# Optimization experiments

Hardware: AMD Instinct MI355X
Metric: run time of the kernel (lower is better)

## Reference

```python
import jax, jax.numpy as jnp
import numpy as np
import math

B, S, CIN, H, W = 8, 8, 64, 32, 32
COUT, K = 128, 3
PW = COUT * CIN * K * K  # 73728
P = PW + COUT            # 73856


def setup_inputs() -> dict:
    key = jax.random.key(0)
    ks = jax.random.split(key, 6)
    return {
        "x": jax.random.normal(ks[0], (B, S, CIN, H, W), dtype=jnp.float32),
        "e": jax.random.normal(ks[1], (S, P), dtype=jnp.float32),
        "mu_w": jax.random.normal(ks[2], (PW,), dtype=jnp.float32) * 0.02,
        "rho_w": jax.random.normal(ks[3], (PW,), dtype=jnp.float32) * 0.5,
        "mu_b": jax.random.normal(ks[4], (COUT,), dtype=jnp.float32) * 0.02,
        "rho_b": jax.random.normal(ks[5], (COUT,), dtype=jnp.float32) * 0.5,
    }


def _unit_log_mfg(v):
    # v: [s_n, D]; -log(2*pi)*D/2 - sum(v**2)/2  (scalar, matching torch code)
    two_pi = jnp.asarray(2.0 * math.pi, v.dtype)
    return -jnp.log(two_pi) * (v.shape[1] / 2.0) - jnp.sum(v * v) / 2.0


def reference(x, e, mu_w, rho_w, mu_b, rho_b):
    s_n = e.shape[0]
    cout = mu_b.shape[0]
    cin = x.shape[2]
    k = int(round(math.sqrt(mu_w.shape[0] / (cout * cin))))
    pw = mu_w.shape[0]

    sig_w = jax.nn.softplus(rho_w)  # log(1+exp(rho))
    sig_b = jax.nn.softplus(rho_b)
    w = mu_w[None, :] + sig_w[None, :] * e[:, :pw]          # [s_n, PW]
    b = mu_b[None, :] + sig_b[None, :] * e[:, pw:pw + cout]  # [s_n, COUT]

    entropy_q = jnp.sum(jnp.log(sig_w)) + jnp.sum(jnp.log(sig_b))
    cross_entropy_qp = _unit_log_mfg(w) + _unit_log_mfg(b)
    kl_qp = -entropy_q - cross_entropy_qp

    w5 = w.reshape(s_n, cout, cin, k, k)  # per-sample OIHW kernels

    # per-sample conv: vmap over the sample axis j; batch conv over data axis i
    def conv_one(xj, wj):  # xj [B,CIN,H,W], wj [COUT,CIN,K,K]
        return jax.lax.conv(xj, wj, (1, 1), 'VALID')

    out = jax.vmap(conv_one, in_axes=(1, 0), out_axes=1)(x, w5)  # [B,S,COUT,H',W']
    out = out + b[None, :, :, None, None]
    return out, kl_qp
```

## Files before the change

kernel.cpp:

```cpp
#include <hip/hip_runtime.h>
#include <hip/hip_bf16.h>
#include <math.h>

#define Bn    8
#define Sn    8
#define COUTc 128
#define PWc   73728
#define Pc    73856
#define WOc   30
#define NPIX  900
#define GPIX  7200
#define NSTEP 9
#define TILE  128
#define NT2   57

typedef __bf16 bf16;
typedef bf16  bf16x8 __attribute__((ext_vector_type(8)));
typedef float f32x16 __attribute__((ext_vector_type(16)));

__device__ __forceinline__ float softplus_f(float x) {
    return fmaxf(x, 0.f) + log1pf(expf(-fabsf(x)));
}

__device__ __forceinline__ unsigned int pack2(float a, float b) {
    unsigned short ua = __builtin_bit_cast(unsigned short, (bf16)a);
    unsigned short ub = __builtin_bit_cast(unsigned short, (bf16)b);
    return ((unsigned int)ub << 16) | (unsigned int)ua;
}

__device__ __forceinline__ void gl16(const void* g, void* l) {
    typedef __attribute__((address_space(1))) void gvoid;
    typedef __attribute__((address_space(3))) void lvoid;
    __builtin_amdgcn_global_load_lds((gvoid*)g, (lvoid*)l, 16, 0, 0);
}

__global__ __launch_bounds__(256) void prep_all(
        const float* __restrict__ xg, const float* __restrict__ e,
        const float* __restrict__ mu_w, const float* __restrict__ rho_w,
        const float* __restrict__ mu_b, const float* __restrict__ rho_b,
        bf16* __restrict__ xt, bf16* __restrict__ wimg,
        float* __restrict__ bq, float* __restrict__ slots) {
    const int bid = blockIdx.x;
    const int t   = threadIdx.x;

    if (bid < 512) {
        const int img  = bid >> 3;
        const int part = bid & 7;
        const int p    = part * 128 + (t >> 1);
        const int half = t & 1;
        const float* src = xg + ((size_t)img << 16) + (size_t)(half * 32) * 1024 + p;
        bf16*        dst = xt + ((size_t)img << 16) + (size_t)p * 64 + half * 32;
        #pragma unroll
        for (int o = 0; o < 4; ++o) {
            uint4 pk;
            pk.x = pack2(src[(o * 8 + 0) * 1024], src[(o * 8 + 1) * 1024]);
            pk.y = pack2(src[(o * 8 + 2) * 1024], src[(o * 8 + 3) * 1024]);
            pk.z = pack2(src[(o * 8 + 4) * 1024], src[(o * 8 + 5) * 1024]);
            pk.w = pack2(src[(o * 8 + 6) * 1024], src[(o * 8 + 7) * 1024]);
            *reinterpret_cast<uint4*>(dst + o * 8) = pk;
        }
        return;
    }

    float ls = 0.f, sq = 0.f;
    if (bid < 800) {
        const int rb    = bid - 512;
        const int r     = rb >> 5;
        const int chunk = rb & 31;
        const int idx   = chunk * 256 + t;
        const int co    = idx >> 6;
        const int ci    = idx & 63;
        const int p     = co * 576 + ci * 9 + r;
        float sig = softplus_f(rho_w[p]);
        ls = logf(sig);
        float mu = mu_w[p];
        const int dstp = (co << 6) + (((ci >> 3) ^ (co & 7)) << 3) + (ci & 7);
        #pragma unroll
        for (int s = 0; s < Sn; ++s) {
            float wv = fmaf(sig, e[s * Pc + p], mu);
            wimg[((s * NSTEP + r) << 13) + dstp] = (bf16)wv;
            sq += wv * wv;
        }
    } else {
        if (t < COUTc) {
            float sig = softplus_f(rho_b[t]);
            ls = logf(sig);
            float mu = mu_b[t];
            #pragma unroll
            for (int s = 0; s < Sn; ++s) {
                float bv = fmaf(sig, e[s * Pc + PWc + t], mu);
                bq[s * COUTc + t] = bv;
                sq += bv * bv;
            }
        }
    }

    #pragma unroll
    for (int off = 32; off > 0; off >>= 1) {
        ls += __shfl_down(ls, off);
        sq += __shfl_down(sq, off);
    }
    __shared__ float sls[4], ssq[4];
    const int lane = t & 63, wd = t >> 6;
    if (lane == 0) { sls[wd] = ls; ssq[wd] = sq; }
    __syncthreads();
    if (t == 0) {
        slots[2 * (bid - 512)]     = sls[0] + sls[1] + sls[2] + sls[3];
        slots[2 * (bid - 512) + 1] = ssq[0] + ssq[1] + ssq[2] + ssq[3];
    }
}

__global__ __launch_bounds__(256) void conv_mfma(
        const bf16* __restrict__ xt, const bf16* __restrict__ wimg,
        const float* __restrict__ bq, const float* __restrict__ slots,
        float* __restrict__ out, float* __restrict__ klout) {
    const int bid  = blockIdx.x;
    const int s    = bid & 7;
    const int tile = bid >> 3;
    const int t    = threadIdx.x;
    const int lane = t & 63;
    const int w    = t >> 6;
    const int wr   = w >> 1;
    const int wc   = w & 1;

    __shared__ bf16 Wbuf[2][8192];
    __shared__ bf16 Xbuf[2][8192];

    const char* wsrcL = (const char*)wimg + ((size_t)(s * NSTEP) << 14)
                      + (w << 12) + (lane << 4);

    const char *x0, *x1, *x2, *x3;
    #pragma unroll
    for (int q = 0; q < 4; ++q) {
        int pix = w * 32 + q * 8 + (lane >> 3);
        int g   = tile * TILE + pix;
        if (g >= GPIX) g = GPIX - 1;
        int b2 = g / NPIX;
        int rr = g - b2 * NPIX;
        int oy = rr / WOc;
        int ox = rr - oy * WOc;
        int m  = (lane & 7) ^ (pix & 7);
        const char* ptr = (const char*)xt
            + ((((size_t)(b2 * Sn + s) << 10) + oy * 32 + ox) << 7) + (m << 4);
        if (q == 0) x0 = ptr; else if (q == 1) x1 = ptr;
        else if (q == 2) x2 = ptr; else x3 = ptr;
    }

    f32x16 acc[2][2];
    #pragma unroll
    for (int i = 0; i < 2; ++i)
        #pragma unroll
        for (int j = 0; j < 2; ++j)
            #pragma unroll
            for (int k = 0; k < 16; ++k)
                acc[i][j][k] = 0.f;

    #define STAGE(stepc, b)                                                  \
    {                                                                        \
        const char* ws_ = wsrcL + ((stepc) << 14);                           \
        char* wl_ = (char*)(&Wbuf[(b)][0]) + (w << 12);                      \
        gl16(ws_,        wl_);                                               \
        gl16(ws_ + 1024, wl_ + 1024);                                        \
        gl16(ws_ + 2048, wl_ + 2048);                                        \
        gl16(ws_ + 3072, wl_ + 3072);                                        \
        const int roff_ = (((stepc) / 3) * 32 + ((stepc) % 3)) * 128;        \
        char* xl_ = (char*)(&Xbuf[(b)][0]) + (w << 12);                      \
        gl16(x0 + roff_, xl_);                                               \
        gl16(x1 + roff_, xl_ + 1024);                                        \
        gl16(x2 + roff_, xl_ + 2048);                                        \
        gl16(x3 + roff_, xl_ + 3072);                                        \
    }

    #define COMPUTE(b)                                                       \
    {                                                                        \
        const bf16* Wl_ = &Wbuf[(b)][0];                                     \
        const bf16* Xl_ = &Xbuf[(b)][0];                                     \
        _Pragma("unroll")                                                    \
        for (int kc = 0; kc < 4; ++kc) {                                     \
            const int oct_ = ((kc << 1) + (lane >> 5)) ^ (lane & 7);         \
            bf16x8 af0 = *reinterpret_cast<const bf16x8*>(                   \
                Wl_ + ((wr * 64 + (lane & 31)) << 6) + (oct_ << 3));         \
            bf16x8 af1 = *reinterpret_cast<const bf16x8*>(                   \
                Wl_ + ((wr * 64 + 32 + (lane & 31)) << 6) + (oct_ << 3));    \
            bf16x8 bf0 = *reinterpret_cast<const bf16x8*>(                   \
                Xl_ + ((wc * 64 + (lane & 31)) << 6) + (oct_ << 3));         \
            bf16x8 bf1 = *reinterpret_cast<const bf16x8*>(                   \
                Xl_ + ((wc * 64 + 32 + (lane & 31)) << 6) + (oct_ << 3));    \
            acc[0][0] = __builtin_amdgcn_mfma_f32_32x32x16_bf16(af0, bf0, acc[0][0], 0, 0, 0); \
            acc[0][1] = __builtin_amdgcn_mfma_f32_32x32x16_bf16(af0, bf1, acc[0][1], 0, 0, 0); \
            acc[1][0] = __builtin_amdgcn_mfma_f32_32x32x16_bf16(af1, bf0, acc[1][0], 0, 0, 0); \
            acc[1][1] = __builtin_amdgcn_mfma_f32_32x32x16_bf16(af1, bf1, acc[1][1], 0, 0, 0); \
        }                                                                    \
    }

    STAGE(0, 0);
    STAGE(1, 1);

    #define ITER(tt, b)                                                      \
        asm volatile("s_waitcnt vmcnt(8)" ::: "memory");                     \
        __builtin_amdgcn_s_barrier();                                        \
        __builtin_amdgcn_sched_barrier(0);                                   \
        COMPUTE(b);                                                          \
        __builtin_amdgcn_sched_barrier(0);                                   \
        __builtin_amdgcn_s_barrier();                                        \
        STAGE((tt) + 2, b);

    ITER(0, 0)
    ITER(1, 1)
    ITER(2, 0)
    ITER(3, 1)
    ITER(4, 0)
    ITER(5, 1)
    ITER(6, 0)
    asm volatile("s_waitcnt vmcnt(8)" ::: "memory");
    __builtin_amdgcn_s_barrier();
    __builtin_amdgcn_sched_barrier(0);
    COMPUTE(1);
    asm volatile("s_waitcnt vmcnt(0)" ::: "memory");
    __builtin_amdgcn_s_barrier();
    __builtin_amdgcn_sched_barrier(0);
    COMPUTE(0);

    #undef ITER
    #undef COMPUTE
    #undef STAGE

    const int colp = lane & 31;
    const int hi   = lane >> 5;
    #pragma unroll
    for (int ti = 0; ti < 2; ++ti) {
        float bs[16];
        #pragma unroll
        for (int reg = 0; reg < 16; ++reg) {
            int co = wr * 64 + ti * 32 + (reg & 3) + 8 * (reg >> 2) + 4 * hi;
            bs[reg] = bq[s * COUTc + co];
        }
        #pragma unroll
        for (int tj = 0; tj < 2; ++tj) {
            int gg = tile * TILE + wc * 64 + tj * 32 + colp;
            if (gg >= GPIX) continue;
            int b2 = gg / NPIX;
            int r2 = gg - b2 * NPIX;
            float* ob = out + (size_t)(b2 * Sn + s) * (COUTc * NPIX) + r2;
            #pragma unroll
            for (int reg = 0; reg < 16; ++reg) {
                int co = wr * 64 + ti * 32 + (reg & 3) + 8 * (reg >> 2) + 4 * hi;
                ob[co * NPIX] = acc[ti][tj][reg] + bs[reg];
            }
        }
    }

    if (bid == 0 && w == 0) {
        float ls = 0.f, sq = 0.f;
        for (int i = lane; i < 289; i += 64) {
            ls += slots[2 * i];
            sq += slots[2 * i + 1];
        }
        #pragma unroll
        for (int off = 32; off > 0; off >>= 1) {
            ls += __shfl_down(ls, off);
            sq += __shfl_down(sq, off);
        }
        if (lane == 0)
            *klout = -ls + 0.91893853320467274f * (float)Pc + 0.5f * sq;
    }
}

extern "C" void kernel_launch(void* const* d_in, const int* in_sizes, int n_in,
                              void* d_out, int out_size, void* d_ws, size_t ws_size,
                              hipStream_t stream) {
    const float* x     = (const float*)d_in[0];
    const float* e     = (const float*)d_in[1];
    const float* mu_w  = (const float*)d_in[2];
    const float* rho_w = (const float*)d_in[3];
    const float* mu_b  = (const float*)d_in[4];
    const float* rho_b = (const float*)d_in[5];
    float* out = (float*)d_out;

    bf16*  wimg  = (bf16*)d_ws;
    float* bq    = (float*)((char*)d_ws + 1179648);
    float* slots = (float*)((char*)d_ws + 1183744);
    bf16*  xt    = (bf16*)((char*)d_ws + 1187840);

    prep_all<<<dim3(801), dim3(256), 0, stream>>>(
        x, e, mu_w, rho_w, mu_b, rho_b, xt, wimg, bq, slots);

    conv_mfma<<<dim3(NT2 * Sn), dim3(256), 0, stream>>>(
        xt, wimg, bq, slots, out, out + (out_size - 1));
}
```

Measured before the change: 30.23 us.

## Use two waves per conv block with larger per-wave tiles; batch weight prep per thread

```diff
diff --git a/kernel.cpp b/kernel.cpp
--- a/kernel.cpp
+++ b/kernel.cpp
@@ -63,23 +63,28 @@
     }
 
     float ls = 0.f, sq = 0.f;
-    if (bid < 800) {
-        const int rb    = bid - 512;
-        const int r     = rb >> 5;
-        const int chunk = rb & 31;
-        const int idx   = chunk * 256 + t;
-        const int co    = idx >> 6;
-        const int ci    = idx & 63;
-        const int p     = co * 576 + ci * 9 + r;
-        float sig = softplus_f(rho_w[p]);
-        ls = logf(sig);
-        float mu = mu_w[p];
+    if (bid < 544) {
+        const int gidx = (bid - 512) * 256 + t;
+        const int co   = gidx >> 6;
+        const int ci   = gidx & 63;
+        const int p0   = co * 576 + ci * 9;
+        float mu[9], sg[9];
+        #pragma unroll
+        for (int r = 0; r < 9; ++r) {
+            mu[r] = mu_w[p0 + r];
+            sg[r] = softplus_f(rho_w[p0 + r]);
+            ls   += logf(sg[r]);
+        }
         const int dstp = (co << 6) + (((ci >> 3) ^ (co & 7)) << 3) + (ci & 7);
         #pragma unroll
         for (int s = 0; s < Sn; ++s) {
-            float wv = fmaf(sig, e[s * Pc + p], mu);
-            wimg[((s * NSTEP + r) << 13) + dstp] = (bf16)wv;
-            sq += wv * wv;
+            const float* es = e + s * Pc + p0;
+            #pragma unroll
+            for (int r = 0; r < 9; ++r) {
+                float wv = fmaf(sg[r], es[r], mu[r]);
+                wimg[((s * NSTEP + r) << 13) + dstp] = (bf16)wv;
+                sq += wv * wv;
+            }
         }
     } else {
         if (t < COUTc) {
@@ -110,7 +115,7 @@
     }
 }
 
-__global__ __launch_bounds__(256) void conv_mfma(
+__global__ __launch_bounds__(128) void conv_mfma(
         const bf16* __restrict__ xt, const bf16* __restrict__ wimg,
         const float* __restrict__ bq, const float* __restrict__ slots,
         float* __restrict__ out, float* __restrict__ klout) {
@@ -120,19 +125,17 @@
     const int t    = threadIdx.x;
     const int lane = t & 63;
     const int w    = t >> 6;
-    const int wr   = w >> 1;
-    const int wc   = w & 1;
 
     __shared__ bf16 Wbuf[2][8192];
     __shared__ bf16 Xbuf[2][8192];
 
     const char* wsrcL = (const char*)wimg + ((size_t)(s * NSTEP) << 14)
-                      + (w << 12) + (lane << 4);
-
-    const char *x0, *x1, *x2, *x3;
-    #pragma unroll
-    for (int q = 0; q < 4; ++q) {
-        int pix = w * 32 + q * 8 + (lane >> 3);
+                      + (w << 13) + (lane << 4);
+
+    const char* xs[8];
+    #pragma unroll
+    for (int q = 0; q < 8; ++q) {
+        int pix = w * 64 + q * 8 + (lane >> 3);
         int g   = tile * TILE + pix;
         if (g >= GPIX) g = GPIX - 1;
         int b2 = g / NPIX;
@@ -140,17 +143,15 @@
         int oy = rr / WOc;
         int ox = rr - oy * WOc;
         int m  = (lane & 7) ^ (pix & 7);
-        const char* ptr = (const char*)xt
+        xs[q] = (const char*)xt
             + ((((size_t)(b2 * Sn + s) << 10) + oy * 32 + ox) << 7) + (m << 4);
-        if (q == 0) x0 = ptr; else if (q == 1) x1 = ptr;
-        else if (q == 2) x2 = ptr; else x3 = ptr;
-    }
-
-    f32x16 acc[2][2];
+    }
+
+    f32x16 acc[2][4];
     #pragma unroll
     for (int i = 0; i < 2; ++i)
         #pragma unroll
-        for (int j = 0; j < 2; ++j)
+        for (int j = 0; j < 4; ++j)
             #pragma unroll
             for (int k = 0; k < 16; ++k)
                 acc[i][j][k] = 0.f;
@@ -158,17 +159,15 @@
     #define STAGE(stepc, b)                                                  \
     {                                                                        \
         const char* ws_ = wsrcL + ((stepc) << 14);                           \
-        char* wl_ = (char*)(&Wbuf[(b)][0]) + (w << 12);                      \
-        gl16(ws_,        wl_);                                               \
-        gl16(ws_ + 1024, wl_ + 1024);                                        \
-        gl16(ws_ + 2048, wl_ + 2048);                                        \
-        gl16(ws_ + 3072, wl_ + 3072);                                        \
+        char* wl_ = (char*)(&Wbuf[(b)][0]) + (w << 13);                      \
+        _Pragma("unroll")                                                    \
+        for (int q = 0; q < 8; ++q)                                          \
+            gl16(ws_ + (q << 10), wl_ + (q << 10));                          \
         const int roff_ = (((stepc) / 3) * 32 + ((stepc) % 3)) * 128;        \
-        char* xl_ = (char*)(&Xbuf[(b)][0]) + (w << 12);                      \
-        gl16(x0 + roff_, xl_);                                               \
-        gl16(x1 + roff_, xl_ + 1024);                                        \
-        gl16(x2 + roff_, xl_ + 2048);                                        \
-        gl16(x3 + roff_, xl_ + 3072);                                        \
+        char* xl_ = (char*)(&Xbuf[(b)][0]) + (w << 13);                      \
+        _Pragma("unroll")                                                    \
+        for (int q = 0; q < 8; ++q)                                          \
+            gl16(xs[q] + roff_, xl_ + (q << 10));                            \
     }
 
     #define COMPUTE(b)                                                       \
@@ -178,18 +177,26 @@
         _Pragma("unroll")                                                    \
         for (int kc = 0; kc < 4; ++kc) {                                     \
             const int oct_ = ((kc << 1) + (lane >> 5)) ^ (lane & 7);         \
-            bf16x8 af0 = *reinterpret_cast<const bf16x8*>(                   \
-                Wl_ + ((wr * 64 + (lane & 31)) << 6) + (oct_ << 3));         \
-            bf16x8 af1 = *reinterpret_cast<const bf16x8*>(                   \
-                Wl_ + ((wr * 64 + 32 + (lane & 31)) << 6) + (oct_ << 3));    \
-            bf16x8 bf0 = *reinterpret_cast<const bf16x8*>(                   \
-                Xl_ + ((wc * 64 + (lane & 31)) << 6) + (oct_ << 3));         \
-            bf16x8 bf1 = *reinterpret_cast<const bf16x8*>(                   \
-                Xl_ + ((wc * 64 + 32 + (lane & 31)) << 6) + (oct_ << 3));    \
-            acc[0][0] = __builtin_amdgcn_mfma_f32_32x32x16_bf16(af0, bf0, acc[0][0], 0, 0, 0); \
-            acc[0][1] = __builtin_amdgcn_mfma_f32_32x32x16_bf16(af0, bf1, acc[0][1], 0, 0, 0); \
-            acc[1][0] = __builtin_amdgcn_mfma_f32_32x32x16_bf16(af1, bf0, acc[1][0], 0, 0, 0); \
-            acc[1][1] = __builtin_amdgcn_mfma_f32_32x32x16_bf16(af1, bf1, acc[1][1], 0, 0, 0); \
+            bf16x8 a0 = *reinterpret_cast<const bf16x8*>(                    \
+                Wl_ + ((w * 64 + (lane & 31)) << 6) + (oct_ << 3));          \
+            bf16x8 a1 = *reinterpret_cast<const bf16x8*>(                    \
+                Wl_ + ((w * 64 + 32 + (lane & 31)) << 6) + (oct_ << 3));     \
+            bf16x8 b0 = *reinterpret_cast<const bf16x8*>(                    \
+                Xl_ + (((lane & 31)) << 6) + (oct_ << 3));                   \
+            bf16x8 b1 = *reinterpret_cast<const bf16x8*>(                    \
+                Xl_ + ((32 + (lane & 31)) << 6) + (oct_ << 3));              \
+            bf16x8 b2 = *reinterpret_cast<const bf16x8*>(                    \
+                Xl_ + ((64 + (lane & 31)) << 6) + (oct_ << 3));              \
+            bf16x8 b3 = *reinterpret_cast<const bf16x8*>(                    \
+                Xl_ + ((96 + (lane & 31)) << 6) + (oct_ << 3));              \
+            acc[0][0] = __builtin_amdgcn_mfma_f32_32x32x16_bf16(a0, b0, acc[0][0], 0, 0, 0); \
+            acc[0][1] = __builtin_amdgcn_mfma_f32_32x32x16_bf16(a0, b1, acc[0][1], 0, 0, 0); \
+            acc[0][2] = __builtin_amdgcn_mfma_f32_32x32x16_bf16(a0, b2, acc[0][2], 0, 0, 0); \
+            acc[0][3] = __builtin_amdgcn_mfma_f32_32x32x16_bf16(a0, b3, acc[0][3], 0, 0, 0); \
+            acc[1][0] = __builtin_amdgcn_mfma_f32_32x32x16_bf16(a1, b0, acc[1][0], 0, 0, 0); \
+            acc[1][1] = __builtin_amdgcn_mfma_f32_32x32x16_bf16(a1, b1, acc[1][1], 0, 0, 0); \
+            acc[1][2] = __builtin_amdgcn_mfma_f32_32x32x16_bf16(a1, b2, acc[1][2], 0, 0, 0); \
+            acc[1][3] = __builtin_amdgcn_mfma_f32_32x32x16_bf16(a1, b3, acc[1][3], 0, 0, 0); \
         }                                                                    \
     }
 
@@ -197,7 +204,7 @@
     STAGE(1, 1);
 
     #define ITER(tt, b)                                                      \
-        asm volatile("s_waitcnt vmcnt(8)" ::: "memory");                     \
+        asm volatile("s_waitcnt vmcnt(16)" ::: "memory");                    \
         __builtin_amdgcn_s_barrier();                                        \
         __builtin_amdgcn_sched_barrier(0);                                   \
         COMPUTE(b);                                                          \
@@ -212,7 +219,7 @@
     ITER(4, 0)
     ITER(5, 1)
     ITER(6, 0)
-    asm volatile("s_waitcnt vmcnt(8)" ::: "memory");
+    asm volatile("s_waitcnt vmcnt(16)" ::: "memory");
     __builtin_amdgcn_s_barrier();
     __builtin_amdgcn_sched_barrier(0);
     COMPUTE(1);
@@ -228,31 +235,31 @@
     const int colp = lane & 31;
     const int hi   = lane >> 5;
     #pragma unroll
-    for (int ti = 0; ti < 2; ++ti) {
+    for (int i = 0; i < 2; ++i) {
         float bs[16];
         #pragma unroll
         for (int reg = 0; reg < 16; ++reg) {
-            int co = wr * 64 + ti * 32 + (reg & 3) + 8 * (reg >> 2) + 4 * hi;
+            int co = w * 64 + i * 32 + (reg & 3) + 8 * (reg >> 2) + 4 * hi;
             bs[reg] = bq[s * COUTc + co];
         }
         #pragma unroll
-        for (int tj = 0; tj < 2; ++tj) {
-            int gg = tile * TILE + wc * 64 + tj * 32 + colp;
+        for (int j = 0; j < 4; ++j) {
+            int gg = tile * TILE + j * 32 + colp;
             if (gg >= GPIX) continue;
             int b2 = gg / NPIX;
             int r2 = gg - b2 * NPIX;
             float* ob = out + (size_t)(b2 * Sn + s) * (COUTc * NPIX) + r2;
             #pragma unroll
             for (int reg = 0; reg < 16; ++reg) {
-                int co = wr * 64 + ti * 32 + (reg & 3) + 8 * (reg >> 2) + 4 * hi;
-                ob[co * NPIX] = acc[ti][tj][reg] + bs[reg];
+                int co = w * 64 + i * 32 + (reg & 3) + 8 * (reg >> 2) + 4 * hi;
+                ob[co * NPIX] = acc[i][j][reg] + bs[reg];
             }
         }
     }
 
     if (bid == 0 && w == 0) {
         float ls = 0.f, sq = 0.f;
-        for (int i = lane; i < 289; i += 64) {
+        for (int i = lane; i < 33; i += 64) {
             ls += slots[2 * i];
             sq += slots[2 * i + 1];
         }
@@ -282,9 +289,9 @@
     float* slots = (float*)((char*)d_ws + 1183744);
     bf16*  xt    = (bf16*)((char*)d_ws + 1187840);
 
-    prep_all<<<dim3(801), dim3(256), 0, stream>>>(
+    prep_all<<<dim3(545), dim3(256), 0, stream>>>(
         x, e, mu_w, rho_w, mu_b, rho_b, xt, wimg, bq, slots);
 
-    conv_mfma<<<dim3(NT2 * Sn), dim3(256), 0, stream>>>(
+    conv_mfma<<<dim3(NT2 * Sn), dim3(128), 0, stream>>>(
         xt, wimg, bq, slots, out, out + (out_size - 1));
 }
```

Result: slower. 35.17 us (+16.4%).

## Halve conv pixel tile and merge weight-prep taps into fewer blocks

Applied to the files above, without the earlier changes.

```diff
diff --git a/kernel.cpp b/kernel.cpp
--- a/kernel.cpp
+++ b/kernel.cpp
@@ -11,8 +11,8 @@
 #define NPIX  900
 #define GPIX  7200
 #define NSTEP 9
-#define TILE  128
-#define NT2   57
+#define TILE  64
+#define NTIL  113
 
 typedef __bf16 bf16;
 typedef bf16  bf16x8 __attribute__((ext_vector_type(8)));
@@ -63,23 +63,28 @@
     }
 
     float ls = 0.f, sq = 0.f;
-    if (bid < 800) {
-        const int rb    = bid - 512;
-        const int r     = rb >> 5;
-        const int chunk = rb & 31;
-        const int idx   = chunk * 256 + t;
-        const int co    = idx >> 6;
-        const int ci    = idx & 63;
-        const int p     = co * 576 + ci * 9 + r;
-        float sig = softplus_f(rho_w[p]);
-        ls = logf(sig);
-        float mu = mu_w[p];
+    if (bid < 544) {
+        const int gidx = (bid - 512) * 256 + t;
+        const int co   = gidx >> 6;
+        const int ci   = gidx & 63;
+        const int p0   = co * 576 + ci * 9;
+        float mu[9], sg[9];
+        #pragma unroll
+        for (int r = 0; r < 9; ++r) {
+            mu[r] = mu_w[p0 + r];
+            sg[r] = softplus_f(rho_w[p0 + r]);
+            ls   += logf(sg[r]);
+        }
         const int dstp = (co << 6) + (((ci >> 3) ^ (co & 7)) << 3) + (ci & 7);
         #pragma unroll
         for (int s = 0; s < Sn; ++s) {
-            float wv = fmaf(sig, e[s * Pc + p], mu);
-            wimg[((s * NSTEP + r) << 13) + dstp] = (bf16)wv;
-            sq += wv * wv;
+            const float* es = e + s * Pc + p0;
+            #pragma unroll
+            for (int r = 0; r < 9; ++r) {
+                float wv = fmaf(sg[r], es[r], mu[r]);
+                wimg[((s * NSTEP + r) << 13) + dstp] = (bf16)wv;
+                sq += wv * wv;
+            }
         }
     } else {
         if (t < COUTc) {
@@ -124,36 +129,30 @@
     const int wc   = w & 1;
 
     __shared__ bf16 Wbuf[2][8192];
-    __shared__ bf16 Xbuf[2][8192];
+    __shared__ bf16 Xbuf[2][4096];
 
     const char* wsrcL = (const char*)wimg + ((size_t)(s * NSTEP) << 14)
                       + (w << 12) + (lane << 4);
 
-    const char *x0, *x1, *x2, *x3;
+    const char *x0, *x1;
     #pragma unroll
-    for (int q = 0; q < 4; ++q) {
-        int pix = w * 32 + q * 8 + (lane >> 3);
+    for (int q = 0; q < 2; ++q) {
+        int pix = w * 16 + q * 8 + (lane >> 3);
         int g   = tile * TILE + pix;
         if (g >= GPIX) g = GPIX - 1;
-        int b2 = g / NPIX;
-        int rr = g - b2 * NPIX;
-        int oy = rr / WOc;
-        int ox = rr - oy * WOc;
+        int b2 = g / NPIX, rr = g - b2 * NPIX, oy = rr / WOc, ox = rr - oy * WOc;
         int m  = (lane & 7) ^ (pix & 7);
         const char* ptr = (const char*)xt
             + ((((size_t)(b2 * Sn + s) << 10) + oy * 32 + ox) << 7) + (m << 4);
-        if (q == 0) x0 = ptr; else if (q == 1) x1 = ptr;
-        else if (q == 2) x2 = ptr; else x3 = ptr;
-    }
-
-    f32x16 acc[2][2];
+        if (q == 0) x0 = ptr; else x1 = ptr;
+    }
+
+    f32x16 acc[2];
     #pragma unroll
     for (int i = 0; i < 2; ++i)
         #pragma unroll
-        for (int j = 0; j < 2; ++j)
-            #pragma unroll
-            for (int k = 0; k < 16; ++k)
-                acc[i][j][k] = 0.f;
+        for (int k = 0; k < 16; ++k)
+            acc[i][k] = 0.f;
 
     #define STAGE(stepc, b)                                                  \
     {                                                                        \
@@ -164,11 +163,9 @@
         gl16(ws_ + 2048, wl_ + 2048);                                        \
         gl16(ws_ + 3072, wl_ + 3072);                                        \
         const int roff_ = (((stepc) / 3) * 32 + ((stepc) % 3)) * 128;        \
-        char* xl_ = (char*)(&Xbuf[(b)][0]) + (w << 12);                      \
+        char* xl_ = (char*)(&Xbuf[(b)][0]) + (w << 11);                      \
         gl16(x0 + roff_, xl_);                                               \
         gl16(x1 + roff_, xl_ + 1024);                                        \
-        gl16(x2 + roff_, xl_ + 2048);                                        \
-        gl16(x3 + roff_, xl_ + 3072);                                        \
     }
 
     #define COMPUTE(b)                                                       \
@@ -183,13 +180,9 @@
             bf16x8 af1 = *reinterpret_cast<const bf16x8*>(                   \
                 Wl_ + ((wr * 64 + 32 + (lane & 31)) << 6) + (oct_ << 3));    \
             bf16x8 bf0 = *reinterpret_cast<const bf16x8*>(                   \
-                Xl_ + ((wc * 64 + (lane & 31)) << 6) + (oct_ << 3));         \
-            bf16x8 bf1 = *reinterpret_cast<const bf16x8*>(                   \
-                Xl_ + ((wc * 64 + 32 + (lane & 31)) << 6) + (oct_ << 3));    \
-            acc[0][0] = __builtin_amdgcn_mfma_f32_32x32x16_bf16(af0, bf0, acc[0][0], 0, 0, 0); \
-            acc[0][1] = __builtin_amdgcn_mfma_f32_32x32x16_bf16(af0, bf1, acc[0][1], 0, 0, 0); \
-            acc[1][0] = __builtin_amdgcn_mfma_f32_32x32x16_bf16(af1, bf0, acc[1][0], 0, 0, 0); \
-            acc[1][1] = __builtin_amdgcn_mfma_f32_32x32x16_bf16(af1, bf1, acc[1][1], 0, 0, 0); \
+                Xl_ + ((wc * 32 + (lane & 31)) << 6) + (oct_ << 3));         \
+            acc[0] = __builtin_amdgcn_mfma_f32_32x32x16_bf16(af0, bf0, acc[0], 0, 0, 0); \
+            acc[1] = __builtin_amdgcn_mfma_f32_32x32x16_bf16(af1, bf0, acc[1], 0, 0, 0); \
         }                                                                    \
     }
 
@@ -197,7 +190,7 @@
     STAGE(1, 1);
 
     #define ITER(tt, b)                                                      \
-        asm volatile("s_waitcnt vmcnt(8)" ::: "memory");                     \
+        asm volatile("s_waitcnt vmcnt(6)" ::: "memory");                     \
         __builtin_amdgcn_s_barrier();                                        \
         __builtin_amdgcn_sched_barrier(0);                                   \
         COMPUTE(b);                                                          \
@@ -212,7 +205,7 @@
     ITER(4, 0)
     ITER(5, 1)
     ITER(6, 0)
-    asm volatile("s_waitcnt vmcnt(8)" ::: "memory");
+    asm volatile("s_waitcnt vmcnt(6)" ::: "memory");
     __builtin_amdgcn_s_barrier();
     __builtin_amdgcn_sched_barrier(0);
     COMPUTE(1);
@@ -227,42 +220,28 @@
 
     const int colp = lane & 31;
     const int hi   = lane >> 5;
-    #pragma unroll
-    for (int ti = 0; ti < 2; ++ti) {
-        float bs[16];
-        #pragma unroll
-        for (int reg = 0; reg < 16; ++reg) {
-            int co = wr * 64 + ti * 32 + (reg & 3) + 8 * (reg >> 2) + 4 * hi;
-            bs[reg] = bq[s * COUTc + co];
-        }
-        #pragma unroll
-        for (int tj = 0; tj < 2; ++tj) {
-            int gg = tile * TILE + wc * 64 + tj * 32 + colp;
-            if (gg >= GPIX) continue;
-            int b2 = gg / NPIX;
-            int r2 = gg - b2 * NPIX;
-            float* ob = out + (size_t)(b2 * Sn + s) * (COUTc * NPIX) + r2;
+    const int gg   = tile * TILE + wc * 32 + colp;
+    if (gg < GPIX) {
+        const int b2 = gg / NPIX;
+        const int r2 = gg - b2 * NPIX;
+        float* ob = out + (size_t)(b2 * Sn + s) * (COUTc * NPIX) + r2;
+        #pragma unroll
+        for (int ti = 0; ti < 2; ++ti) {
             #pragma unroll
             for (int reg = 0; reg < 16; ++reg) {
                 int co = wr * 64 + ti * 32 + (reg & 3) + 8 * (reg >> 2) + 4 * hi;
-                ob[co * NPIX] = acc[ti][tj][reg] + bs[reg];
+                ob[co * NPIX] = acc[ti][reg] + bq[s * COUTc + co];
             }
         }
     }
 
-    if (bid == 0 && w == 0) {
+    if (bid == 0 && t == 0) {
         float ls = 0.f, sq = 0.f;
-        for (int i = lane; i < 289; i += 64) {
-            ls += slots[2 * i];
-            sq += slots[2 * i + 1];
-        }
-        #pragma unroll
-        for (int off = 32; off > 0; off >>= 1) {
-            ls += __shfl_down(ls, off);
-            sq += __shfl_down(sq, off);
-        }
-        if (lane == 0)
-            *klout = -ls + 0.91893853320467274f * (float)Pc + 0.5f * sq;
+        for (int i2 = 0; i2 < 33; ++i2) {
+            ls += slots[2 * i2];
+            sq += slots[2 * i2 + 1];
+        }
+        *klout = -ls + 0.91893853320467274f * (float)Pc + 0.5f * sq;
     }
 }
 
@@ -282,9 +261,9 @@
     float* slots = (float*)((char*)d_ws + 1183744);
     bf16*  xt    = (bf16*)((char*)d_ws + 1187840);
 
-    prep_all<<<dim3(801), dim3(256), 0, stream>>>(
+    prep_all<<<dim3(545), dim3(256), 0, stream>>>(
         x, e, mu_w, rho_w, mu_b, rho_b, xt, wimg, bq, slots);
 
-    conv_mfma<<<dim3(NT2 * Sn), dim3(256), 0, stream>>>(
+    conv_mfma<<<dim3(NTIL * Sn), dim3(256), 0, stream>>>(
         xt, wimg, bq, slots, out, out + (out_size - 1));
 }
```

New measurement: 35.93 us. +18.9%, slower.
